# Kernel optimization log

Hardware: AMD Instinct MI355X
Metric: run time of the kernel (lower is better)

Reference implementation:

```python
import jax, jax.numpy as jnp
import numpy as np

EMBED_LEN = 512
NUM_FEA = 8   # M
NUM_CLS = 14  # C
BETA = 0.3
BATCH = 8192


def setup_inputs() -> dict:
    key = jax.random.key(0)
    k1, k2, k3 = jax.random.split(key, 3)
    x = jax.random.normal(k1, (BATCH, EMBED_LEN * NUM_FEA), dtype=jnp.float32)
    wordvec_array = jax.random.normal(k2, (1, EMBED_LEN, NUM_CLS), dtype=jnp.float32)
    y = jax.random.randint(k3, (BATCH, NUM_CLS), 0, 2, dtype=jnp.int32)
    # guarantee at least one positive and one negative label per sample
    y = y.at[:, 0].set(1).at[:, -1].set(0)
    return {"x": x, "y": y, "wordvec_array": wordvec_array}


def reference(x, y, wordvec_array):
    B = x.shape[0]
    un = x.reshape(B, EMBED_LEN, -1)            # [B, E, M]
    w = wordvec_array[0]                         # [E, C]
    # dot_prod_all[b, c] = max_m <un[b,:,m], w[:,c]>
    dot = jnp.einsum('bem,ec->bmc', un, w).max(axis=1)   # [B, C]

    P = (y == 1).astype(x.dtype)                 # positive mask [B, C]
    N = 1.0 - P                                  # negative mask [B, C]
    npos = P.sum(axis=-1)                        # [B]
    nneg = N.sum(axis=-1)                        # [B]

    # pairwise v[b,p,n] = dot_neg - dot_pos; sum softplus over masked pairs
    V = dot[:, None, :] - dot[:, :, None]        # [B, C(pos), C(neg)]
    pair_sum = jnp.einsum('bp,bn,bpn->b', P, N, jax.nn.softplus(V))
    # edge case: no negatives -> v = -dot_pos
    noneg_sum = jnp.sum(P * jax.nn.softplus(-dot), axis=-1)
    S = jnp.where(nneg > 0, pair_sum, noneg_sum)
    base = S / npos                              # [B]

    # diversity: unbiased variance of positive-class word vectors over class dim
    mean_w = jnp.einsum('bc,ec->be', P, w) / npos[:, None]          # [B, E]
    ss = jnp.einsum('bc,bec->be', P, (w[None] - mean_w[:, :, None]) ** 2)
    var_w = ss / jnp.maximum(npos - 1.0, 1.0)[:, None]
    var_w = jnp.where((npos == 1.0)[:, None], 0.0, var_w)           # sig = 0 if single positive
    total_var = var_w.sum(axis=-1)               # [B]

    # var_regularization: unbiased var over M, L1 over embed dim
    sig2 = jnp.var(un, axis=2, ddof=1)           # [B, E]
    l1_err = jnp.abs(sig2).sum(axis=-1)          # [B]

    # num_fea > 1 branch
    loss = 2.0 * ((1.0 - BETA) * (1.0 + total_var) * base + BETA * l1_err)
    return loss.mean()
```

## Files before the change

### kernel.cpp

```cpp
#include <hip/hip_runtime.h>
#include <math.h>

#define E_LEN 512
#define C_CLS 14
#define BATCH 8192
#define NSLOTS 256
#define WS_G 256
#define WS_WB 464
#define WB_ROW 260

typedef float v4f __attribute__((ext_vector_type(4)));
typedef short s8v __attribute__((ext_vector_type(8)));
union APk { int i[4]; s8v s; };

#define CVT_PK_BF16(d, a, b) \
  asm("v_cvt_pk_bf16_f32 %0, %1, %2" : "=v"(d) : "v"(a), "v"(b))

template<int CTRL>
__device__ __forceinline__ float dpp_mov_f(float v) {
  return __int_as_float(__builtin_amdgcn_update_dpp(
      0, __float_as_int(v), CTRL, 0xF, 0xF, false));
}
__device__ __forceinline__ float sum16(float v) {
  v += dpp_mov_f<0x128>(v);
  v += dpp_mov_f<0x124>(v);
  v += dpp_mov_f<0x122>(v);
  v += dpp_mov_f<0x121>(v);
  return v;
}
__device__ __forceinline__ float hsum32(float v) {
  v = sum16(v);
  v += dpp_mov_f<0x142>(v);
  return v;
}
__device__ __forceinline__ float wsum64(float v) {
  v = sum16(v);
  v += dpp_mov_f<0x142>(v);
  v += dpp_mov_f<0x143>(v);
  return v;
}
template<int PAT>
__device__ __forceinline__ float swz_f(float v) {
  return __int_as_float(__builtin_amdgcn_ds_swizzle(__float_as_int(v), PAT));
}
__device__ __forceinline__ float shfl_x32(float v) {
  return __shfl_xor(v, 32, 64);
}
__device__ __forceinline__ float softplus_f(float v) {
  return fmaxf(v, 0.f) + __logf(1.f + __expf(-fabsf(v)));
}

__global__ void MID_LOSS_prep(const float* __restrict__ w,
                              float* __restrict__ wsf) {
  __shared__ float wl[E_LEN * C_CLS];
  const int tid = threadIdx.x;
#pragma unroll
  for (int i = 0; i < 7; ++i)
    ((float4*)wl)[tid + i * 256] = ((const float4*)w)[tid + i * 256];
  wsf[tid] = 0.f;
  __syncthreads();
  if (tid < 196) {
    const int p = tid / 14, n = tid - p * 14;
    float g = 0.f;
    for (int e = 0; e < E_LEN; ++e)
      g = fmaf(wl[e * 14 + p], wl[e * 14 + n], g);
    wsf[WS_G + tid] = g;
  }
  unsigned int* wsu = (unsigned int*)wsf;
  for (int i = tid; i < 4096; i += 256) {
    const int c = i >> 8;
    const int ep = i & 255;
    const int e = ep * 2;
    const float v0 = (c < 14) ? wl[e * 14 + c] : 0.f;
    const float v1 = (c < 14) ? wl[(e + 1) * 14 + c] : 0.f;
    int d;
    CVT_PK_BF16(d, v0, v1);
    wsu[WS_WB + c * WB_ROW + ep] = (unsigned int)d;
  }
}

__global__ __launch_bounds__(256, 4)
void MID_LOSS_main(const float* __restrict__ x, const int* __restrict__ y,
                   const float* __restrict__ wsf, float* __restrict__ slots) {
  __shared__ unsigned int wB_l[16 * WB_ROW];
  __shared__ float G_l[196];
  __shared__ float dots_l[4][2][16];
  __shared__ float P_l[4][2][16];

  const int tid = threadIdx.x;
  const int lane = tid & 63;
  const int wid = tid >> 6;
  const unsigned int* wsu = (const unsigned int*)wsf;

  for (int i = tid; i < 16 * WB_ROW; i += 256) wB_l[i] = wsu[WS_WB + i];
  if (tid < 196) G_l[tid] = wsf[WS_G + tid];
  __syncthreads();

  const int row = lane & 15;
  const int kg = lane >> 4;
  const int b0 = blockIdx.x * 8 + wid * 2;
  const int b = b0 + (row >> 3);
  const int m = row & 7;
  const float* xp = x + (size_t)b * (E_LEN * 8) + kg * 64 + m;

  v4f acc = {0.f, 0.f, 0.f, 0.f};
  v4f acc2 = {0.f, 0.f, 0.f, 0.f};
  float q = 0.f;
#pragma unroll
  for (int ch = 0; ch < 16; ++ch) {
    const float* xc = xp + ch * 256;
    float u[8];
#pragma unroll
    for (int j = 0; j < 8; ++j) u[j] = xc[j * 8];
#pragma unroll
    for (int j = 0; j < 8; ++j) q = fmaf(u[j], u[j], q);
    APk a;
#pragma unroll
    for (int jj = 0; jj < 4; ++jj) CVT_PK_BF16(a.i[jj], u[2 * jj], u[2 * jj + 1]);
    const s8v bfrag =
        *(const s8v*)(wB_l + (lane & 15) * WB_ROW + ch * 16 + kg * 4);
    acc = __builtin_amdgcn_mfma_f32_16x16x32_bf16(a.s, bfrag, acc, 0, 0, 0);
    acc2 = __builtin_amdgcn_mfma_f32_16x16x32_bf16(a.s, a.s, acc2, 0, 0, 0);
  }

  if (lane < 28) {
    const int s = (lane >= 14) ? 1 : 0;
    P_l[wid][s][lane - s * 14] = (y[b0 * 14 + lane] == 1) ? 1.f : 0.f;
  }

  float dmax = fmaxf(fmaxf(acc[0], acc[1]), fmaxf(acc[2], acc[3]));
  dmax = fmaxf(dmax, swz_f<0x401F>(dmax));
  if ((lane & 16) == 0 && (lane & 15) < 14)
    dots_l[wid][lane >> 5][lane & 15] = dmax;

  const float loc2 = acc2[0] + acc2[1] + acc2[2] + acc2[3];
  const bool validb = (((lane & 15) < 8) == (lane < 32));
  float s2v = validb ? loc2 : 0.f;
  float q2 = q + shfl_x32(q);
  float qv = validb ? q2 : 0.f;

  asm volatile("s_waitcnt lgkmcnt(0)" ::: "memory");

  const int half = lane >> 5;
  const int hl = lane & 31;
  const float* dp = dots_l[wid][half];
  const float* Pp = P_l[wid][half];
  float S = 0.f, Gc = 0.f;
#pragma unroll
  for (int r = 0; r < 7; ++r) {
    const int tt = r * 28 + hl;
    if (hl < 28) {
      const int p = (tt * 2341) >> 15;
      const int n = tt - p * 14;
      const float Ppv = Pp[p], Pnv = Pp[n];
      S += Ppv * (1.f - Pnv) * softplus_f(dp[n] - dp[p]);
      Gc = fmaf(Ppv * Pnv, G_l[tt], Gc);
    }
  }
  float npv = (hl < 14) ? Pp[hl] : 0.f;
  float w2v = (hl < 14) ? Pp[hl] * G_l[hl * 15] : 0.f;

  S = hsum32(S);
  Gc = hsum32(Gc);
  s2v = hsum32(s2v);
  qv = hsum32(qv);
  npv = hsum32(npv);
  w2v = hsum32(w2v);

  float loss = 0.f;
  if ((lane & 31) == 31) {
    const float npos = npv;
    const float base = S / npos;
    const float tv =
        (npos > 1.5f) ? (w2v - Gc / npos) / (npos - 1.f) : 0.f;
    const float l1 = (qv - s2v * 0.125f) * (1.f / 7.f);
    loss = 1.4f * (1.f + tv) * base + 0.6f * l1;
  }
  loss += shfl_x32(loss);
  if (lane == 31) atomicAdd(&slots[blockIdx.x & (NSLOTS - 1)], loss);
}

__global__ void MID_LOSS_fin(const float* __restrict__ wsf,
                             float* __restrict__ out) {
  const int tid = threadIdx.x;
  float s = wsf[tid] + wsf[tid + 64] + wsf[tid + 128] + wsf[tid + 192];
  s = wsum64(s);
  if (tid == 63) out[0] = s * (1.f / (float)BATCH);
}

extern "C" void kernel_launch(void* const* d_in, const int* in_sizes, int n_in,
                              void* d_out, int out_size, void* d_ws, size_t ws_size,
                              hipStream_t stream) {
  const float* x = (const float*)d_in[0];
  const int* y = (const int*)d_in[1];
  const float* w = (const float*)d_in[2];
  float* out = (float*)d_out;
  float* wsf = (float*)d_ws;

  MID_LOSS_prep<<<1, 256, 0, stream>>>(w, wsf);
  MID_LOSS_main<<<BATCH / 8, 256, 0, stream>>>(x, y, wsf, wsf);
  MID_LOSS_fin<<<1, 64, 0, stream>>>(wsf, out);
}
```

Baseline: 216.8 us.

## Stream x into LDS via global_load_lds double buffering

Replaces the strided direct global loads of x (8-element stride per lane) with coalesced global_load_lds DMA into a per-wave double-buffered LDS staging area, prefetching two chunks ahead. The aim is to coalesce memory access and overlap HBM traffic with the MFMA work. It adds about 18 KB of LDS per block, which may reduce occupancy, and it depends on hand-placed vmcnt/lgkmcnt waits being correct.

New measurement: 212.1 us. 2.2% less time.

```diff
diff --git a/kernel.cpp b/kernel.cpp
--- a/kernel.cpp
+++ b/kernel.cpp
@@ -8,6 +8,11 @@
 #define WS_G 256
 #define WS_WB 464
 #define WB_ROW 260
+#define NCH 16
+#define XKG 72
+#define XSLOT 288
+#define XBUF 576
+#define XW 1152
 
 typedef float v4f __attribute__((ext_vector_type(4)));
 typedef short s8v __attribute__((ext_vector_type(8)));
@@ -15,6 +20,12 @@
 
 #define CVT_PK_BF16(d, a, b) \
   asm("v_cvt_pk_bf16_f32 %0, %1, %2" : "=v"(d) : "v"(a), "v"(b))
+
+__device__ __forceinline__ void dma4(const float* gp, float* lp) {
+  __builtin_amdgcn_global_load_lds(
+      (const __attribute__((address_space(1))) void*)gp,
+      (__attribute__((address_space(3))) void*)lp, 4, 0, 0);
+}
 
 template<int CTRL>
 __device__ __forceinline__ float dpp_mov_f(float v) {
@@ -84,6 +95,7 @@
                    const float* __restrict__ wsf, float* __restrict__ slots) {
   __shared__ unsigned int wB_l[16 * WB_ROW];
   __shared__ float G_l[196];
+  __shared__ alignas(16) float xs[4 * XW];
   __shared__ float dots_l[4][2][16];
   __shared__ float P_l[4][2][16];
 
@@ -98,27 +110,56 @@
 
   const int row = lane & 15;
   const int kg = lane >> 4;
+  const int m = row & 7;
   const int b0 = blockIdx.x * 8 + wid * 2;
-  const int b = b0 + (row >> 3);
-  const int m = row & 7;
-  const float* xp = x + (size_t)b * (E_LEN * 8) + kg * 64 + m;
+  const float* xg = x + (size_t)b0 * 4096;
+  float* xw = xs + wid * XW;
+  const float* xr = xw + (row >> 3) * XSLOT + kg * XKG + m;
+  const unsigned int* wrow = wB_l + row * WB_ROW;
+
+#pragma unroll
+  for (int c = 0; c < 2; ++c)
+#pragma unroll
+    for (int sl = 0; sl < 2; ++sl)
+#pragma unroll
+      for (int kk = 0; kk < 4; ++kk)
+        dma4(xg + sl * 4096 + c * 256 + kk * 64 + lane,
+             xw + c * XBUF + sl * XSLOT + kk * XKG);
 
   v4f acc = {0.f, 0.f, 0.f, 0.f};
   v4f acc2 = {0.f, 0.f, 0.f, 0.f};
   float q = 0.f;
-#pragma unroll
-  for (int ch = 0; ch < 16; ++ch) {
-    const float* xc = xp + ch * 256;
+
+#pragma unroll
+  for (int ch = 0; ch < NCH; ++ch) {
+    const int buf = ch & 1;
+    if (ch == NCH - 1)
+      asm volatile("s_waitcnt vmcnt(0)" ::: "memory");
+    else
+      asm volatile("s_waitcnt vmcnt(8)" ::: "memory");
+
     float u[8];
-#pragma unroll
-    for (int j = 0; j < 8; ++j) u[j] = xc[j * 8];
+    const float* xb = xr + buf * XBUF;
+#pragma unroll
+    for (int j = 0; j < 8; ++j) u[j] = xb[j * 8];
+    const s8v bfrag = *(const s8v*)(wrow + ch * 16 + kg * 4);
 #pragma unroll
     for (int j = 0; j < 8; ++j) q = fmaf(u[j], u[j], q);
     APk a;
 #pragma unroll
-    for (int jj = 0; jj < 4; ++jj) CVT_PK_BF16(a.i[jj], u[2 * jj], u[2 * jj + 1]);
-    const s8v bfrag =
-        *(const s8v*)(wB_l + (lane & 15) * WB_ROW + ch * 16 + kg * 4);
+    for (int jj = 0; jj < 4; ++jj)
+      CVT_PK_BF16(a.i[jj], u[2 * jj], u[2 * jj + 1]);
+
+    if (ch < NCH - 2) {
+      asm volatile("s_waitcnt lgkmcnt(0)" ::: "memory");
+#pragma unroll
+      for (int sl = 0; sl < 2; ++sl)
+#pragma unroll
+        for (int kk = 0; kk < 4; ++kk)
+          dma4(xg + sl * 4096 + (ch + 2) * 256 + kk * 64 + lane,
+               xw + buf * XBUF + sl * XSLOT + kk * XKG);
+    }
+
     acc = __builtin_amdgcn_mfma_f32_16x16x32_bf16(a.s, bfrag, acc, 0, 0, 0);
     acc2 = __builtin_amdgcn_mfma_f32_16x16x32_bf16(a.s, a.s, acc2, 0, 0, 0);
   }
```
